# Performance work log

Measured on AMD Instinct MI355X. Metric: run time of the kernel, lower is better.

Reference implementation:

```python
import math
import jax, jax.numpy as jnp
import numpy as np

D_MODEL = 512
NHEAD = 8
FACTOR = 5


def setup_inputs() -> dict:
    key = jax.random.key(0)
    ks = jax.random.split(key, 16)
    B, L, D = 4, 2048, D_MODEL
    s = 0.02
    inp = {
        "queries": jax.random.normal(ks[0], (B, L, D), jnp.float32),
        "keys": jax.random.normal(ks[1], (B, L, D), jnp.float32),
        "values": jax.random.normal(ks[2], (B, L, D), jnp.float32),
        "Wq": jax.random.normal(ks[3], (D, D), jnp.float32) * s,
        "bq": jnp.zeros((D,), jnp.float32),
        "Wk": jax.random.normal(ks[4], (D, D), jnp.float32) * s,
        "bk": jnp.zeros((D,), jnp.float32),
        "Wv": jax.random.normal(ks[5], (D, D), jnp.float32) * s,
        "bv": jnp.zeros((D,), jnp.float32),
        "Wo": jax.random.normal(ks[6], (D, D), jnp.float32) * s,
        "bo": jnp.zeros((D,), jnp.float32),
    }
    # sample_k = factor * ceil(ln(L_K+1)) = 5*8 = 40, shared across batch & heads
    U = min(FACTOR * int(np.ceil(np.log(L + 1))), L)
    inp["index_sample"] = jax.random.randint(ks[7], (L, U), 0, L, jnp.int32)
    return inp


def reference(queries, keys, values, Wq, bq, Wk, bk, Wv, bv, Wo, bo, index_sample):
    B, LQ, D = queries.shape
    LK = keys.shape[1]
    H = NHEAD
    dk = D // H

    # projections (torch Linear: x @ W.T + b), split into heads -> (B,H,L,dk)
    def proj(x, W, b):
        y = x @ W.T + b
        return y.reshape(B, -1, H, dk).transpose(0, 2, 1, 3)

    Q = proj(queries, Wq, bq)
    K = proj(keys, Wk, bk)
    V = proj(values, Wv, bv)

    U = min(FACTOR * int(np.ceil(np.log(LK + 1))), LK)  # sampled keys per query
    u = min(FACTOR * int(np.ceil(np.log(LQ + 1))), LQ)  # top queries kept

    # initial context: mean of V broadcast over queries  (B,H,LQ,dk)
    context = jnp.broadcast_to(V.mean(axis=2, keepdims=True), (B, H, LQ, dk))

    if LQ > u:
        # gather sampled keys: (B,H,LQ,U,dk)  [dominant memory traffic]
        K_sample = K[:, :, index_sample, :]
        # per-query scores against sampled keys: (B,H,LQ,U)
        QK_sample = jnp.einsum('bhqd,bhqud->bhqu', Q, K_sample)
        # sparsity measure M = max - mean
        M = QK_sample.max(axis=-1) - QK_sample.sum(axis=-1) / LK  # (B,H,LQ)
        M_top = jax.lax.top_k(M, u)[1]  # (B,H,u)

        # gather selected queries: (B,H,u,dk)
        Q_reduce = jnp.take_along_axis(Q, M_top[..., None], axis=2)
        scores = jnp.einsum('bhud,bhkd->bhuk', Q_reduce, K) / math.sqrt(dk)
        attn = jax.nn.softmax(scores, axis=-1)  # dropout = eval mode (identity)
        context_in = jnp.einsum('bhuk,bhkd->bhud', attn, V)  # (B,H,u,dk)

        # scatter attended rows back into the mean context
        bi = jnp.arange(B)[:, None, None]
        hi = jnp.arange(H)[None, :, None]
        context = context.at[bi, hi, M_top].set(context_in)
    else:
        scores = jnp.einsum('bhqd,bhkd->bhqk', Q, K) / math.sqrt(dk)
        attn = jax.nn.softmax(scores, axis=-1)
        context = jnp.einsum('bhqk,bhkd->bhqd', attn, V)

    context = context.transpose(0, 2, 1, 3).reshape(B, LQ, D)
    return context @ Wo.T + bo
```

## Files before the change

### kernel.cpp

```cpp
#include <hip/hip_runtime.h>
#include <math.h>

constexpr int Bn  = 4;
constexpr int Ln  = 2048;
constexpr int Dn  = 512;
constexpr int Hn  = 8;
constexpr int DKn = 64;
constexpr int US  = 40;
constexpr int UT  = 40;
constexpr int NCk = 32;
constexpr int CKn = 64;

typedef unsigned short ushort_t;

__device__ __forceinline__ ushort_t f2bf_rne(float x) {
  unsigned u = __float_as_uint(x);
  unsigned r = u + 0x7fffu + ((u >> 16) & 1u);
  return (ushort_t)(r >> 16);
}
__device__ __forceinline__ float bf2f(ushort_t h) {
  return __uint_as_float(((unsigned)h) << 16);
}

__global__ __launch_bounds__(256) void split_in(const float* __restrict__ X,
                                                ushort_t* __restrict__ A)
{
  int i = blockIdx.x * 256 + threadIdx.x;
  int m = i >> 7, c4 = (i & 127) << 2;
  float4 x = *reinterpret_cast<const float4*>(&X[(size_t)m * 512 + c4]);
  ushort_t h0 = f2bf_rne(x.x), h1 = f2bf_rne(x.y), h2 = f2bf_rne(x.z), h3 = f2bf_rne(x.w);
  ushort_t l0 = f2bf_rne(x.x - bf2f(h0)), l1 = f2bf_rne(x.y - bf2f(h1));
  ushort_t l2 = f2bf_rne(x.z - bf2f(h2)), l3 = f2bf_rne(x.w - bf2f(h3));
  *reinterpret_cast<ushort4*>(&A[(size_t)m * 1024 + c4])       = make_ushort4(h0, h1, h2, h3);
  *reinterpret_cast<ushort4*>(&A[(size_t)m * 1024 + 512 + c4]) = make_ushort4(l0, l1, l2, l3);
}

__global__ __launch_bounds__(256) void split_w(const float* __restrict__ W,
                                               ushort_t* __restrict__ Wc)
{
  int i = blockIdx.x * 256 + threadIdx.x;
  int n = i >> 7, c4 = (i & 127) << 2;
  float4 x = *reinterpret_cast<const float4*>(&W[(size_t)n * 512 + c4]);
  ushort_t h0 = f2bf_rne(x.x), h1 = f2bf_rne(x.y), h2 = f2bf_rne(x.z), h3 = f2bf_rne(x.w);
  ushort_t l0 = f2bf_rne(x.x - bf2f(h0)), l1 = f2bf_rne(x.y - bf2f(h1));
  ushort_t l2 = f2bf_rne(x.z - bf2f(h2)), l3 = f2bf_rne(x.w - bf2f(h3));
  ushort4 hv = make_ushort4(h0, h1, h2, h3);
  ushort4 lv = make_ushort4(l0, l1, l2, l3);
  *reinterpret_cast<ushort4*>(&Wc[(size_t)n * 1536 + c4])        = hv;
  *reinterpret_cast<ushort4*>(&Wc[(size_t)n * 1536 + 512 + c4])  = lv;
  *reinterpret_cast<ushort4*>(&Wc[(size_t)n * 1536 + 1024 + c4]) = hv;
}

using bf16x8 = short __attribute__((ext_vector_type(8)));
using f32x4  = float __attribute__((ext_vector_type(4)));

__device__ __forceinline__ void gload_lds16(const void* g, void* l) {
  __builtin_amdgcn_global_load_lds((const __attribute__((address_space(1))) void*)g,
                                   (__attribute__((address_space(3))) void*)l, 16, 0, 0);
}

__global__ __launch_bounds__(256) void gemm3_bf16(const ushort_t* __restrict__ Ast,
    const ushort_t* __restrict__ Bst, const float* __restrict__ bias,
    float* __restrict__ out)
{
  __shared__ __attribute__((aligned(16))) ushort_t sA[64 * 64];
  __shared__ __attribute__((aligned(16))) ushort_t sB[128 * 64];
  const int tid = threadIdx.x;
  const int w = tid >> 6, lane = tid & 63;
  const int m0 = blockIdx.y * 64, n0 = blockIdx.x * 128;
  const int wr = w >> 1, wc = w & 1;
  const int r16 = lane & 15, ko = (lane >> 4) * 8;

  f32x4 acc[2][4];
#pragma unroll
  for (int m = 0; m < 2; ++m)
#pragma unroll
    for (int n = 0; n < 4; ++n) acc[m][n] = (f32x4){0.f, 0.f, 0.f, 0.f};

  for (int k0 = 0; k0 < 1536; k0 += 64) {
    const int ka0 = (k0 < 1024) ? (k0 & 511) : (k0 - 512);
    __syncthreads();
#pragma unroll
    for (int i = 0; i < 2; ++i) {
      int e = i * 256 + tid, r = e >> 3, c8 = e & 7;
      gload_lds16(Ast + (size_t)(m0 + r) * 1024 + ka0 + c8 * 8,
                  (void*)(sA + (size_t)(i * 256 + w * 64) * 8));
    }
#pragma unroll
    for (int i = 0; i < 4; ++i) {
      int e = i * 256 + tid, r = e >> 3, c8 = e & 7;
      gload_lds16(Bst + (size_t)(n0 + r) * 1536 + k0 + c8 * 8,
                  (void*)(sB + (size_t)(i * 256 + w * 64) * 8));
    }
    __syncthreads();
#pragma unroll
    for (int kk = 0; kk < 64; kk += 32) {
      bf16x8 a[2], b[4];
#pragma unroll
      for (int m = 0; m < 2; ++m)
        a[m] = *reinterpret_cast<const bf16x8*>(&sA[(wr * 32 + m * 16 + r16) * 64 + kk + ko]);
#pragma unroll
      for (int n = 0; n < 4; ++n)
        b[n] = *reinterpret_cast<const bf16x8*>(&sB[(wc * 64 + n * 16 + r16) * 64 + kk + ko]);
#pragma unroll
      for (int m = 0; m < 2; ++m)
#pragma unroll
        for (int n = 0; n < 4; ++n)
          acc[m][n] = __builtin_amdgcn_mfma_f32_16x16x32_bf16(a[m], b[n], acc[m][n], 0, 0, 0);
    }
  }

#pragma unroll
  for (int m = 0; m < 2; ++m) {
#pragma unroll
    for (int n = 0; n < 4; ++n) {
#pragma unroll
      for (int r = 0; r < 4; ++r) {
        int row = m0 + wr * 32 + m * 16 + (lane >> 4) * 4 + r;
        int col = n0 + wc * 64 + n * 16 + (lane & 15);
        float v = acc[m][n][r] + bias[col];
        int b = row >> 11, l = row & 2047, h = col >> 6, dd = col & 63;
        out[(size_t)((b * Hn + h) * Ln + l) * DKn + dd] = v;
      }
    }
  }
}

__global__ __launch_bounds__(256) void vmean1(const float* __restrict__ Vf,
                                              float* __restrict__ part)
{
  int bh = blockIdx.x, ch = blockIdx.y;
  int t = threadIdx.x;
  int d4 = t & 15, ls = t >> 4;
  const float* base = Vf + ((size_t)bh * Ln + ch * 128) * DKn;
  float4 s = make_float4(0.f, 0.f, 0.f, 0.f);
#pragma unroll
  for (int i = 0; i < 8; ++i) {
    float4 x = *reinterpret_cast<const float4*>(&base[(size_t)(ls + i * 16) * DKn + d4 * 4]);
    s.x += x.x; s.y += x.y; s.z += x.z; s.w += x.w;
  }
  __shared__ float4 red[16][16];
  red[ls][d4] = s;
  __syncthreads();
  if (t < 64) {
    int dd = t & 15, g = t >> 4;
    float4 a = red[g * 4 + 0][dd], b = red[g * 4 + 1][dd];
    float4 c = red[g * 4 + 2][dd], d = red[g * 4 + 3][dd];
    red[g * 4][dd] = make_float4(a.x + b.x + c.x + d.x, a.y + b.y + c.y + d.y,
                                 a.z + b.z + c.z + d.z, a.w + b.w + c.w + d.w);
  }
  __syncthreads();
  if (t < 16) {
    float4 a = red[0][t], b = red[4][t], c = red[8][t], d = red[12][t];
    float4 r = make_float4(a.x + b.x + c.x + d.x, a.y + b.y + c.y + d.y,
                           a.z + b.z + c.z + d.z, a.w + b.w + c.w + d.w);
    *reinterpret_cast<float4*>(&part[((size_t)(bh * 16 + ch)) * DKn + t * 4]) = r;
  }
}

__global__ __launch_bounds__(64) void vmean2(const float* __restrict__ part,
                                             float* __restrict__ meanV)
{
  int bh = blockIdx.x, d = threadIdx.x;
  float s = 0.f;
#pragma unroll
  for (int ch = 0; ch < 16; ++ch) s += part[((size_t)(bh * 16 + ch)) * DKn + d];
  meanV[bh * DKn + d] = s * (1.f / 2048.f);
}

__global__ __launch_bounds__(256) void qk_sample_m2(const float* __restrict__ Qf,
    const float* __restrict__ Kf, const int* __restrict__ isamp,
    float* __restrict__ Mout)
{
  int wq = blockIdx.x * 4 + (threadIdx.x >> 6);
  int lane = threadIdx.x & 63;
  int g = lane >> 4, s = lane & 15;
  int bh = wq >> 11, q = wq & 2047;
  const float* Kb = Kf + (size_t)bh * Ln * DKn;
  float4 qv = *reinterpret_cast<const float4*>(&Qf[(size_t)(bh * Ln + q) * DKn + s * 4]);
  float mx = -INFINITY, sm = 0.f;
#pragma unroll
  for (int p = 0; p < 10; ++p) {
    int u = p * 4 + g;
    int idx = isamp[q * US + u];
    float4 kv = *reinterpret_cast<const float4*>(&Kb[(size_t)idx * DKn + s * 4]);
    float d = qv.x * kv.x + qv.y * kv.y + qv.z * kv.z + qv.w * kv.w;
#pragma unroll
    for (int off = 1; off < 16; off <<= 1) d += __shfl_xor(d, off);
    mx = fmaxf(mx, d);
    sm += d;
  }
#pragma unroll
  for (int off = 16; off <= 32; off <<= 1) {
    mx = fmaxf(mx, __shfl_xor(mx, off));
    sm += __shfl_xor(sm, off);
  }
  if (lane == 0) Mout[wq] = mx - sm * (1.f / 2048.f);
}

__global__ __launch_bounds__(256) void topk40(const float* __restrict__ Mv,
                                              int* __restrict__ Mtop)
{
  int bh = blockIdx.x, tid = threadIdx.x;
  __shared__ unsigned hist[256];
  __shared__ unsigned sfx[256];
  __shared__ unsigned prefix_s, k_s;
  __shared__ int outcnt, tiecnt;
  __shared__ int tlist[256];

  unsigned key[8];
#pragma unroll
  for (int i = 0; i < 8; ++i) {
    unsigned u = __float_as_uint(Mv[bh * Ln + tid + i * 256]);
    key[i] = (u & 0x80000000u) ? ~u : (u | 0x80000000u);
  }
  if (tid == 0) { prefix_s = 0u; k_s = UT; outcnt = 0; tiecnt = 0; }
  __syncthreads();

  for (int d = 24; d >= 0; d -= 8) {
    hist[tid] = 0u;
    __syncthreads();
    unsigned pref = prefix_s;
    unsigned mask = (d == 24) ? 0u : (0xFFFFFFFFu << (d + 8));
#pragma unroll
    for (int i = 0; i < 8; ++i)
      if ((key[i] & mask) == pref) atomicAdd(&hist[(key[i] >> d) & 255u], 1u);
    __syncthreads();
    sfx[tid] = hist[tid];
    __syncthreads();
    for (int off = 1; off < 256; off <<= 1) {
      unsigned add = (tid + off < 256) ? sfx[tid + off] : 0u;
      __syncthreads();
      sfx[tid] += add;
      __syncthreads();
    }
    unsigned k = k_s;
    unsigned nxt = (tid < 255) ? sfx[tid + 1] : 0u;
    if (sfx[tid] >= k && nxt < k) {
      prefix_s = pref | ((unsigned)tid << d);
      k_s = k - nxt;
    }
    __syncthreads();
  }

  unsigned T = prefix_s;
  int kf = (int)k_s;
#pragma unroll
  for (int i = 0; i < 8; ++i) {
    int idx = tid + i * 256;
    if (key[i] > T) {
      int s = atomicAdd(&outcnt, 1);
      Mtop[bh * UT + s] = idx;
    } else if (key[i] == T) {
      int s = atomicAdd(&tiecnt, 1);
      if (s < 256) tlist[s] = idx;
    }
  }
  __syncthreads();
  if (tid == 0) {
    int n = tiecnt < 256 ? tiecnt : 256;
    int basep = outcnt;
    for (int a = 0; a < kf; ++a) {
      int best = 1 << 30, bj = 0;
      for (int j = 0; j < n; ++j)
        if (tlist[j] < best) { best = tlist[j]; bj = j; }
      Mtop[bh * UT + basep + a] = best;
      tlist[bj] = 1 << 30;
    }
  }
}

__global__ __launch_bounds__(256) void attn_partial(const float* __restrict__ Qf,
    const float* __restrict__ Kf, const float* __restrict__ Vf,
    const int* __restrict__ Mtop, float* __restrict__ pmv,
    float* __restrict__ plv, float* __restrict__ pacc)
{
  const int bh = blockIdx.x, c = blockIdx.y;
  const int tid = threadIdx.x;
  const int w = tid >> 6, lane = tid & 63;
  __shared__ float sQ[UT][DKn];
  __shared__ float sS[UT][CKn];
  __shared__ float sK[CKn * DKn];

  for (int i = tid; i < UT * DKn; i += 256) {
    int r = i >> 6, d = i & 63;
    sQ[r][d] = Qf[(size_t)(bh * Ln + Mtop[bh * UT + r]) * DKn + d];
  }
  const float* Kc = Kf + (size_t)(bh * Ln + c * CKn) * DKn;
  for (int i = tid; i < CKn * DKn; i += 256) {
    int r = i >> 6, d = i & 63;
    sK[r * 64 + (d ^ ((r & 15) << 2))] = Kc[(size_t)r * DKn + d];
  }
  __syncthreads();

  for (int it = 0; it < 10; ++it) {
    int i = w + it * 4, kk = lane;
    float s = 0.f;
#pragma unroll
    for (int g = 0; g < 16; ++g) {
      float4 qv = *reinterpret_cast<const float4*>(&sQ[i][g * 4]);
      float4 kv = *reinterpret_cast<const float4*>(&sK[kk * 64 + ((g * 4) ^ ((kk & 15) << 2))]);
      s += qv.x * kv.x + qv.y * kv.y + qv.z * kv.z + qv.w * kv.w;
    }
    sS[i][kk] = s * 0.125f;
  }
  __syncthreads();

  for (int it = 0; it < 10; ++it) {
    int i = w + it * 4;
    float s0 = sS[i][lane];
    float mx = s0;
#pragma unroll
    for (int off = 32; off; off >>= 1) mx = fmaxf(mx, __shfl_xor(mx, off));
    float p0 = expf(s0 - mx);
    sS[i][lane] = p0;
    float ls = p0;
#pragma unroll
    for (int off = 32; off; off >>= 1) ls += __shfl_xor(ls, off);
    if (lane == 0) {
      pmv[(bh * NCk + c) * UT + i] = mx;
      plv[(bh * NCk + c) * UT + i] = ls;
    }
  }
  __syncthreads();

  const int ksub = lane >> 4, dq = lane & 15;
  const float* Vc = Vf + (size_t)(bh * Ln + c * CKn) * DKn;
  float4 acc[10];
#pragma unroll
  for (int t = 0; t < 10; ++t) acc[t] = make_float4(0.f, 0.f, 0.f, 0.f);
  for (int ko = 0; ko < 16; ++ko) {
    int kk = ko * 4 + ksub;
    float4 v4 = *reinterpret_cast<const float4*>(&Vc[(size_t)kk * DKn + dq * 4]);
#pragma unroll
    for (int t = 0; t < 10; ++t) {
      float wgt = sS[w + t * 4][kk];
      acc[t].x += wgt * v4.x; acc[t].y += wgt * v4.y;
      acc[t].z += wgt * v4.z; acc[t].w += wgt * v4.w;
    }
  }
#pragma unroll
  for (int t = 0; t < 10; ++t) {
#pragma unroll
    for (int off = 16; off <= 32; off <<= 1) {
      acc[t].x += __shfl_xor(acc[t].x, off);
      acc[t].y += __shfl_xor(acc[t].y, off);
      acc[t].z += __shfl_xor(acc[t].z, off);
      acc[t].w += __shfl_xor(acc[t].w, off);
    }
  }
  if (ksub == 0) {
#pragma unroll
    for (int t = 0; t < 10; ++t) {
      int i = w + t * 4;
      *reinterpret_cast<float4*>(&pacc[(size_t)((bh * NCk + c) * UT + i) * DKn + dq * 4]) = acc[t];
    }
  }
}

__global__ __launch_bounds__(256) void base_proj(const float* __restrict__ meanV,
    const float* __restrict__ Wo, const float* __restrict__ bo,
    float* __restrict__ base)
{
  int b = blockIdx.x, tid = threadIdx.x;
#pragma unroll
  for (int rep = 0; rep < 2; ++rep) {
    int n = tid + rep * 256;
    float s = bo[n];
#pragma unroll 8
    for (int g = 0; g < 128; ++g) {
      float4 wv = *reinterpret_cast<const float4*>(&Wo[(size_t)n * Dn + g * 4]);
      float4 mv = *reinterpret_cast<const float4*>(&meanV[b * Dn + g * 4]);
      s += wv.x * mv.x + wv.y * mv.y + wv.z * mv.z + wv.w * mv.w;
    }
    base[b * Dn + n] = s;
  }
}

__global__ __launch_bounds__(256) void base_fill(const float* __restrict__ base,
                                                 float* __restrict__ out)
{
  int idx = blockIdx.x * 256 + threadIdx.x;
  int row = idx >> 7, col4 = idx & 127;
  int b = row >> 11;
  reinterpret_cast<float4*>(out)[idx] =
      reinterpret_cast<const float4*>(base)[b * 128 + col4];
}

__global__ __launch_bounds__(256) void combine_ctx(const float* __restrict__ pmv,
    const float* __restrict__ plv, const float* __restrict__ pacc,
    const float* __restrict__ meanV, float* __restrict__ ctxd)
{
  int bh = blockIdx.x, tid = threadIdx.x;
  __shared__ float ew[UT][NCk];
  __shared__ float den_s[UT];
  if (tid < UT) {
    float mg = -INFINITY;
#pragma unroll
    for (int cc = 0; cc < NCk; ++cc)
      mg = fmaxf(mg, pmv[(bh * NCk + cc) * UT + tid]);
    float den = 0.f;
#pragma unroll
    for (int cc = 0; cc < NCk; ++cc) {
      float e = expf(pmv[(bh * NCk + cc) * UT + tid] - mg);
      ew[tid][cc] = e;
      den += plv[(bh * NCk + cc) * UT + tid] * e;
    }
    den_s[tid] = den;
  }
  __syncthreads();
  for (int v = tid; v < UT * DKn; v += 256) {
    int i = v >> 6, d = v & 63;
    float num = 0.f;
#pragma unroll
    for (int cc = 0; cc < NCk; ++cc)
      num += ew[i][cc] * pacc[(size_t)((bh * NCk + cc) * UT + i) * DKn + d];
    ctxd[(size_t)(bh * UT + i) * DKn + d] = num / den_s[i] - meanV[bh * DKn + d];
  }
}

__global__ __launch_bounds__(256) void scatter_proj(const float* __restrict__ ctxd,
    const int* __restrict__ Mtop, const float* __restrict__ Wo,
    float* __restrict__ out)
{
  int nc = blockIdx.x, bh = blockIdx.y;
  int b = bh >> 3, h = bh & 7;
  int tid = threadIdx.x;
  __shared__ float sd[UT][DKn];
  __shared__ int qidx[UT];
  for (int v = tid; v < UT * DKn; v += 256)
    sd[v >> 6][v & 63] = ctxd[(size_t)(bh * UT) * DKn + v];
  if (tid < UT) qidx[tid] = Mtop[bh * UT + tid];
  __syncthreads();

  int n = nc * 64 + (tid & 63);
  int i0 = tid >> 6;
  const float* Wrow = Wo + (size_t)n * Dn + h * DKn;
  float4 wv[16];
#pragma unroll
  for (int g = 0; g < 16; ++g)
    wv[g] = *reinterpret_cast<const float4*>(&Wrow[g * 4]);

#pragma unroll
  for (int t = 0; t < 10; ++t) {
    int i = i0 + t * 4;
    float s = 0.f;
#pragma unroll
    for (int g = 0; g < 16; ++g) {
      float4 dv = *reinterpret_cast<const float4*>(&sd[i][g * 4]);
      s += wv[g].x * dv.x + wv[g].y * dv.y + wv[g].z * dv.z + wv[g].w * dv.w;
    }
    atomicAdd(&out[(size_t)(b * Ln + qidx[i]) * Dn + n], s);
  }
}

extern "C" void kernel_launch(void* const* d_in, const int* in_sizes, int n_in,
                              void* d_out, int out_size, void* d_ws, size_t ws_size,
                              hipStream_t stream)
{
  const float* queries = (const float*)d_in[0];
  const float* keys    = (const float*)d_in[1];
  const float* values  = (const float*)d_in[2];
  const float* Wq = (const float*)d_in[3];
  const float* bq = (const float*)d_in[4];
  const float* Wk = (const float*)d_in[5];
  const float* bk = (const float*)d_in[6];
  const float* Wv = (const float*)d_in[7];
  const float* bv = (const float*)d_in[8];
  const float* Wo = (const float*)d_in[9];
  const float* bo = (const float*)d_in[10];
  const int* isamp = (const int*)d_in[11];
  float* out = (float*)d_out;

  float* ws = (float*)d_ws;
  const size_t NBL = (size_t)Bn * Hn * Ln * DKn;
  float* Qf    = ws;
  float* Kf    = Qf + NBL;
  float* Vf    = Kf + NBL;
  float* meanV = Vf + NBL;
  float* Mv    = meanV + Bn * Hn * DKn;
  float* pmv   = Mv + Bn * Hn * Ln;
  float* plv   = pmv + Bn * Hn * NCk * UT;
  float* base  = plv + Bn * Hn * NCk * UT;
  int* Mtop    = (int*)(base + Bn * Dn);
  float* ctxd  = (float*)(Mtop + Bn * Hn * UT);
  ushort_t* Acat = (ushort_t*)(ctxd + (size_t)Bn * Hn * UT * DKn);
  ushort_t* Wcat = Acat + (size_t)8192 * 1024;
  float* vpart = (float*)(Wcat + (size_t)512 * 1536);
  float* pacc  = (float*)Acat;

  dim3 gg(4, 128);
  split_in<<<4096, 256, 0, stream>>>(queries, Acat);
  split_w<<<256, 256, 0, stream>>>(Wq, Wcat);
  gemm3_bf16<<<gg, 256, 0, stream>>>(Acat, Wcat, bq, Qf);
  split_in<<<4096, 256, 0, stream>>>(keys, Acat);
  split_w<<<256, 256, 0, stream>>>(Wk, Wcat);
  gemm3_bf16<<<gg, 256, 0, stream>>>(Acat, Wcat, bk, Kf);
  split_in<<<4096, 256, 0, stream>>>(values, Acat);
  split_w<<<256, 256, 0, stream>>>(Wv, Wcat);
  gemm3_bf16<<<gg, 256, 0, stream>>>(Acat, Wcat, bv, Vf);

  vmean1<<<dim3(Bn * Hn, 16), 256, 0, stream>>>(Vf, vpart);
  vmean2<<<Bn * Hn, 64, 0, stream>>>(vpart, meanV);
  qk_sample_m2<<<Bn * Hn * Ln / 4, 256, 0, stream>>>(Qf, Kf, isamp, Mv);
  topk40<<<Bn * Hn, 256, 0, stream>>>(Mv, Mtop);
  attn_partial<<<dim3(Bn * Hn, NCk), 256, 0, stream>>>(Qf, Kf, Vf, Mtop, pmv, plv, pacc);
  base_proj<<<Bn, 256, 0, stream>>>(meanV, Wo, bo, base);
  base_fill<<<4096, 256, 0, stream>>>(base, out);
  combine_ctx<<<Bn * Hn, 256, 0, stream>>>(pmv, plv, pacc, meanV, ctxd);
  scatter_proj<<<dim3(8, Bn * Hn), 256, 0, stream>>>(ctxd, Mtop, Wo, out);
}
```

Baseline: 355.2 us.

## Batch Q/K/V split and projection GEMMs into single 3D-grid launches

```diff
diff --git a/kernel.cpp b/kernel.cpp
--- a/kernel.cpp
+++ b/kernel.cpp
@@ -22,22 +22,30 @@
   return __uint_as_float(((unsigned)h) << 16);
 }
 
-__global__ __launch_bounds__(256) void split_in(const float* __restrict__ X,
-                                                ushort_t* __restrict__ A)
-{
+__global__ __launch_bounds__(256) void split_in3(const float* __restrict__ X0,
+    const float* __restrict__ X1, const float* __restrict__ X2,
+    ushort_t* __restrict__ A)
+{
+  int z = blockIdx.y;
+  const float* X = (z == 0) ? X0 : ((z == 1) ? X1 : X2);
+  ushort_t* Az = A + (size_t)z * 8192 * 1024;
   int i = blockIdx.x * 256 + threadIdx.x;
   int m = i >> 7, c4 = (i & 127) << 2;
   float4 x = *reinterpret_cast<const float4*>(&X[(size_t)m * 512 + c4]);
   ushort_t h0 = f2bf_rne(x.x), h1 = f2bf_rne(x.y), h2 = f2bf_rne(x.z), h3 = f2bf_rne(x.w);
   ushort_t l0 = f2bf_rne(x.x - bf2f(h0)), l1 = f2bf_rne(x.y - bf2f(h1));
   ushort_t l2 = f2bf_rne(x.z - bf2f(h2)), l3 = f2bf_rne(x.w - bf2f(h3));
-  *reinterpret_cast<ushort4*>(&A[(size_t)m * 1024 + c4])       = make_ushort4(h0, h1, h2, h3);
-  *reinterpret_cast<ushort4*>(&A[(size_t)m * 1024 + 512 + c4]) = make_ushort4(l0, l1, l2, l3);
-}
-
-__global__ __launch_bounds__(256) void split_w(const float* __restrict__ W,
-                                               ushort_t* __restrict__ Wc)
-{
+  *reinterpret_cast<ushort4*>(&Az[(size_t)m * 1024 + c4])       = make_ushort4(h0, h1, h2, h3);
+  *reinterpret_cast<ushort4*>(&Az[(size_t)m * 1024 + 512 + c4]) = make_ushort4(l0, l1, l2, l3);
+}
+
+__global__ __launch_bounds__(256) void split_w3(const float* __restrict__ W0,
+    const float* __restrict__ W1, const float* __restrict__ W2,
+    ushort_t* __restrict__ Wc)
+{
+  int z = blockIdx.y;
+  const float* W = (z == 0) ? W0 : ((z == 1) ? W1 : W2);
+  ushort_t* Wz = Wc + (size_t)z * 512 * 1536;
   int i = blockIdx.x * 256 + threadIdx.x;
   int n = i >> 7, c4 = (i & 127) << 2;
   float4 x = *reinterpret_cast<const float4*>(&W[(size_t)n * 512 + c4]);
@@ -46,9 +54,9 @@
   ushort_t l2 = f2bf_rne(x.z - bf2f(h2)), l3 = f2bf_rne(x.w - bf2f(h3));
   ushort4 hv = make_ushort4(h0, h1, h2, h3);
   ushort4 lv = make_ushort4(l0, l1, l2, l3);
-  *reinterpret_cast<ushort4*>(&Wc[(size_t)n * 1536 + c4])        = hv;
-  *reinterpret_cast<ushort4*>(&Wc[(size_t)n * 1536 + 512 + c4])  = lv;
-  *reinterpret_cast<ushort4*>(&Wc[(size_t)n * 1536 + 1024 + c4]) = hv;
+  *reinterpret_cast<ushort4*>(&Wz[(size_t)n * 1536 + c4])        = hv;
+  *reinterpret_cast<ushort4*>(&Wz[(size_t)n * 1536 + 512 + c4])  = lv;
+  *reinterpret_cast<ushort4*>(&Wz[(size_t)n * 1536 + 1024 + c4]) = hv;
 }
 
 using bf16x8 = short __attribute__((ext_vector_type(8)));
@@ -59,10 +67,17 @@
                                    (__attribute__((address_space(3))) void*)l, 16, 0, 0);
 }
 
-__global__ __launch_bounds__(256) void gemm3_bf16(const ushort_t* __restrict__ Ast,
-    const ushort_t* __restrict__ Bst, const float* __restrict__ bias,
-    float* __restrict__ out)
-{
+__global__ __launch_bounds__(256) void gemm3_bf16_all(const ushort_t* __restrict__ AcatAll,
+    const ushort_t* __restrict__ WcatAll, const float* __restrict__ bq,
+    const float* __restrict__ bk, const float* __restrict__ bv,
+    float* __restrict__ QKVf)
+{
+  const int z = blockIdx.z;
+  const ushort_t* Ast = AcatAll + (size_t)z * 8192 * 1024;
+  const ushort_t* Bst = WcatAll + (size_t)z * 512 * 1536;
+  const float* bias = (z == 0) ? bq : ((z == 1) ? bk : bv);
+  float* out = QKVf + (size_t)z * Bn * Hn * Ln * DKn;
+
   __shared__ __attribute__((aligned(16))) ushort_t sA[64 * 64];
   __shared__ __attribute__((aligned(16))) ushort_t sB[128 * 64];
   const int tid = threadIdx.x;
@@ -278,14 +293,11 @@
   const int bh = blockIdx.x, c = blockIdx.y;
   const int tid = threadIdx.x;
   const int w = tid >> 6, lane = tid & 63;
-  __shared__ float sQ[UT][DKn];
   __shared__ float sS[UT][CKn];
   __shared__ float sK[CKn * DKn];
-
-  for (int i = tid; i < UT * DKn; i += 256) {
-    int r = i >> 6, d = i & 63;
-    sQ[r][d] = Qf[(size_t)(bh * Ln + Mtop[bh * UT + r]) * DKn + d];
-  }
+  __shared__ int qidx[UT];
+
+  if (tid < UT) qidx[tid] = Mtop[bh * UT + tid];
   const float* Kc = Kf + (size_t)(bh * Ln + c * CKn) * DKn;
   for (int i = tid; i < CKn * DKn; i += 256) {
     int r = i >> 6, d = i & 63;
@@ -293,12 +305,14 @@
   }
   __syncthreads();
 
+  const float* Qb = Qf + (size_t)bh * Ln * DKn;
   for (int it = 0; it < 10; ++it) {
     int i = w + it * 4, kk = lane;
+    const float* Qrow = Qb + (size_t)qidx[i] * DKn;
     float s = 0.f;
 #pragma unroll
     for (int g = 0; g < 16; ++g) {
-      float4 qv = *reinterpret_cast<const float4*>(&sQ[i][g * 4]);
+      float4 qv = *reinterpret_cast<const float4*>(&Qrow[g * 4]);
       float4 kv = *reinterpret_cast<const float4*>(&sK[kk * 64 + ((g * 4) ^ ((kk & 15) << 2))]);
       s += qv.x * kv.x + qv.y * kv.y + qv.z * kv.z + qv.w * kv.w;
     }
@@ -484,21 +498,14 @@
   float* base  = plv + Bn * Hn * NCk * UT;
   int* Mtop    = (int*)(base + Bn * Dn);
   float* ctxd  = (float*)(Mtop + Bn * Hn * UT);
-  ushort_t* Acat = (ushort_t*)(ctxd + (size_t)Bn * Hn * UT * DKn);
-  ushort_t* Wcat = Acat + (size_t)8192 * 1024;
-  float* vpart = (float*)(Wcat + (size_t)512 * 1536);
-  float* pacc  = (float*)Acat;
-
-  dim3 gg(4, 128);
-  split_in<<<4096, 256, 0, stream>>>(queries, Acat);
-  split_w<<<256, 256, 0, stream>>>(Wq, Wcat);
-  gemm3_bf16<<<gg, 256, 0, stream>>>(Acat, Wcat, bq, Qf);
-  split_in<<<4096, 256, 0, stream>>>(keys, Acat);
-  split_w<<<256, 256, 0, stream>>>(Wk, Wcat);
-  gemm3_bf16<<<gg, 256, 0, stream>>>(Acat, Wcat, bk, Kf);
-  split_in<<<4096, 256, 0, stream>>>(values, Acat);
-  split_w<<<256, 256, 0, stream>>>(Wv, Wcat);
-  gemm3_bf16<<<gg, 256, 0, stream>>>(Acat, Wcat, bv, Vf);
+  ushort_t* AcatAll = (ushort_t*)(ctxd + (size_t)Bn * Hn * UT * DKn);
+  ushort_t* WcatAll = AcatAll + (size_t)3 * 8192 * 1024;
+  float* vpart = (float*)(WcatAll + (size_t)3 * 512 * 1536);
+  float* pacc  = (float*)AcatAll;
+
+  split_in3<<<dim3(4096, 3), 256, 0, stream>>>(queries, keys, values, AcatAll);
+  split_w3<<<dim3(256, 3), 256, 0, stream>>>(Wq, Wk, Wv, WcatAll);
+  gemm3_bf16_all<<<dim3(4, 128, 3), 256, 0, stream>>>(AcatAll, WcatAll, bq, bk, bv, Qf);
 
   vmean1<<<dim3(Bn * Hn, 16), 256, 0, stream>>>(Vf, vpart);
   vmean2<<<Bn * Hn, 64, 0, stream>>>(vpart, meanV);
```

After: 327.5 us. 1.08x faster.
